# Performance work log

Hardware: AMD Instinct MI355X
Metric: run time of the kernel (lower is better)

Reference implementation:

```python
import jax, jax.numpy as jnp
import numpy as np
from jax import lax

B, T, O, E, I = 256, 16, 32, 32, 32
H, HL = 64, 64  # edge_dim, latent_edge_dim
TE, EI = T * E, E + I


def _mlp(x, layers):
    for w, b in layers[:-1]:
        x = jax.nn.relu(x @ w + b)
    w, b = layers[-1]
    return x @ w + b


def _get_edges(x, layers):
    # x: [B, O, D]; antisymmetric pairwise aggregation over upper-triangular pairs
    Bn, On, D = x.shape
    ii, jj = np.triu_indices(On, 1)  # static indices, P = O(O-1)/2
    pair_in = jnp.concatenate([x[:, ii, :], x[:, jj, :]], axis=-1)  # [B, P, 2D]
    e = _mlp(pair_in, layers)  # [B, P, H_out]
    agg = jnp.zeros((Bn, On, e.shape[-1]), x.dtype)
    agg = agg.at[:, ii, :].add(e).at[:, jj, :].add(-e)
    return agg


def setup_inputs() -> dict:
    key = jax.random.key(0)
    ks = iter(jax.random.split(key, 64))

    def lin(din, dout):
        w = jax.random.normal(next(ks), (din, dout), jnp.float32) * (1.0 / np.sqrt(din)).astype(np.float32)
        b = jnp.zeros((dout,), jnp.float32)
        return w, b

    inp = {"z_explicit_seq": jax.random.normal(next(ks), (B, T, O, E), jnp.float32)}
    groups = {
        "ee": [(2 * TE, 64), (64, 64), (64, H)],
        "ne": [(TE + H, 64), (64, 64), (64, 32), (32, I)],
        "le": [(2 * EI, 64), (64, 64), (64, HL)],
        "lt": [(EI + HL, 64), (64, 64), (64, 32), (32, 16), (16, EI)],
    }
    for name, dims in groups.items():
        for k, (din, dout) in enumerate(dims, start=1):
            w, b = lin(din, dout)
            inp[f"{name}{k}_w"] = w
            inp[f"{name}{k}_b"] = b
    inp["t_future"] = 8
    return inp


def reference(z_explicit_seq,
              ee1_w, ee1_b, ee2_w, ee2_b, ee3_w, ee3_b,
              ne1_w, ne1_b, ne2_w, ne2_b, ne3_w, ne3_b, ne4_w, ne4_b,
              le1_w, le1_b, le2_w, le2_b, le3_w, le3_b,
              lt1_w, lt1_b, lt2_w, lt2_b, lt3_w, lt3_b, lt4_w, lt4_b, lt5_w, lt5_b,
              t_future):
    ee = [(ee1_w, ee1_b), (ee2_w, ee2_b), (ee3_w, ee3_b)]
    ne = [(ne1_w, ne1_b), (ne2_w, ne2_b), (ne3_w, ne3_b), (ne4_w, ne4_b)]
    le = [(le1_w, le1_b), (le2_w, le2_b), (le3_w, le3_b)]
    lt = [(lt1_w, lt1_b), (lt2_w, lt2_b), (lt3_w, lt3_b), (lt4_w, lt4_b), (lt5_w, lt5_b)]

    z = z_explicit_seq  # [B, T, O, E]
    # define_source: first frame + temporal diffs, flatten time into features
    src = jnp.concatenate([z[:, :1], z[:, 1:] - z[:, :-1]], axis=1)  # [B,T,O,E]
    src = jnp.transpose(src, (0, 2, 1, 3)).reshape(B, O, TE)  # [B,O,TE]

    edge_agg = _get_edges(src, ee)  # [B,O,H]
    z_impl = _mlp(jnp.concatenate([src, edge_agg], axis=-1), ne)  # [B,O,I]
    z_cur = jnp.concatenate([z[:, -1], z_impl], axis=-1)  # [B,O,EI]

    def step(zc, _):
        agg = _get_edges(zc, le)  # [B,O,HL]
        delta = _mlp(jnp.concatenate([zc, agg], axis=-1), lt)  # [B,O,EI]
        zn = zc + delta
        return zn, zn[..., :E]

    _, preds = lax.scan(step, z_cur, None, length=t_future)  # [t,B,O,E]
    return jnp.transpose(preds, (1, 0, 2, 3))  # [B,t_future,O,E]
```

## Files before the change

kernel.cpp:

```cpp
#include <hip/hip_runtime.h>

#define NB 256
#define NO 32
#define NEE 32
#define NT 16
#define THREADS 512

typedef const float* __restrict__ fp;

struct Params {
  fp z;
  fp ee1w, ee1b, ee2w, ee2b, ee3w, ee3b;
  fp ne1w, ne1b, ne2w, ne2b, ne3w, ne3b, ne4w, ne4b;
  fp le1w, le1b, le2w, le2b, le3w, le3b;
  fp lt1w, lt1b, lt2w, lt2b, lt3w, lt3b, lt4w, lt4b, lt5w, lt5b;
  float* out;
  int tf;
};

__device__ __forceinline__ float frelu(float x) { return x > 0.f ? x : 0.f; }

__device__ __forceinline__ float rl(float v, int l) {
  return __uint_as_float(__builtin_amdgcn_readlane(__float_as_uint(v), l));
}

#define OFF_UT  0
#define OFF_VT  2112
#define OFF_AG  4224
#define OFF_BN  6272
#define OFF_NW  8320
#define LDSF    16000

__device__ __forceinline__ void stageN(float* dst, const float* __restrict__ src,
                                       int nf4, int tid) {
  for (int i4 = tid; i4 < nf4; i4 += THREADS)
    *(float4*)(dst + i4 * 4) = *(const float4*)(src + i4 * 4);
}

template<int KC>
__device__ __forceinline__ void dense4L(const float* x0, const float* x1,
                                        const float* x2, const float* x3,
                                        const float* __restrict__ w, int ldw,
                                        int col, float o[4]) {
#pragma unroll 4
  for (int kc = 0; kc < KC; ++kc) {
    float w0 = w[(4 * kc + 0) * ldw + col];
    float w1 = w[(4 * kc + 1) * ldw + col];
    float w2 = w[(4 * kc + 2) * ldw + col];
    float w3 = w[(4 * kc + 3) * ldw + col];
    float4 a = *(const float4*)(x0 + 4 * kc);
    float4 b = *(const float4*)(x1 + 4 * kc);
    float4 c = *(const float4*)(x2 + 4 * kc);
    float4 d = *(const float4*)(x3 + 4 * kc);
    o[0] = fmaf(a.x, w0, o[0]); o[0] = fmaf(a.y, w1, o[0]); o[0] = fmaf(a.z, w2, o[0]); o[0] = fmaf(a.w, w3, o[0]);
    o[1] = fmaf(b.x, w0, o[1]); o[1] = fmaf(b.y, w1, o[1]); o[1] = fmaf(b.z, w2, o[1]); o[1] = fmaf(b.w, w3, o[1]);
    o[2] = fmaf(c.x, w0, o[2]); o[2] = fmaf(c.y, w1, o[2]); o[2] = fmaf(c.z, w2, o[2]); o[2] = fmaf(c.w, w3, o[2]);
    o[3] = fmaf(d.x, w0, o[3]); o[3] = fmaf(d.y, w1, o[3]); o[3] = fmaf(d.z, w2, o[3]); o[3] = fmaf(d.w, w3, o[3]);
  }
}

__global__ __attribute__((amdgpu_waves_per_eu(2)))
__launch_bounds__(THREADS) void rld_kernel(Params P) {
  __shared__ float lds[LDSF];
  const int b = blockIdx.x;
  const int tid = (int)threadIdx.x;
  const int lane = tid & 63;
  const int wave = tid >> 6;
  const int cc = lane & 31;
  const int c16 = lane & 15;

  float* UT = lds + OFF_UT;
  float* VT = lds + OFF_VT;
  float* AG = lds + OFF_AG;
  float* sBn = lds + OFF_BN + wave * 256;
  float* src = lds + OFF_BN;
  const float* wlt2 = lds + OFF_NW;
  const float* wlt3 = lds + OFF_NW + 4096;
  const float* wlt4 = lds + OFF_NW + 6144;
  const float* wlt5 = lds + OFF_NW + 6656;
  const int i0 = wave, i1 = wave + 8, i2 = wave + 16, i3 = wave + 24;
  const int h33 = lane * 33;
  const float* zb = P.z + (size_t)b * NT * NO * NEE;

  stageN(lds + OFF_NW,        P.lt2w, 1024, tid);
  stageN(lds + OFF_NW + 4096, P.lt3w,  512, tid);
  stageN(lds + OFF_NW + 6144, P.lt4w,  128, tid);
  stageN(lds + OFF_NW + 6656, P.lt5w,  256, tid);

  float au[4] = {0,0,0,0}, av[4] = {0,0,0,0}, s1r[4] = {0,0,0,0};
  for (int qq = 0; qq < 8; ++qq) {
    __syncthreads();
    for (int idx = tid; idx < 2048; idx += THREADS) {
      int i = idx >> 6, kk = idx & 63;
      int k = qq * 64 + kk, t = k >> 5, e = k & 31;
      float v = zb[(t * NO + i) * NEE + e];
      if (t > 0) v -= zb[((t - 1) * NO + i) * NEE + e];
      src[i * 64 + kk] = v;
    }
    __syncthreads();
    for (int c = 0; c < 2; ++c) {
      int r0 = qq * 64 + c * 32;
      const float* x0 = src + i0 * 64 + c * 32;
      const float* x1 = src + i1 * 64 + c * 32;
      const float* x2 = src + i2 * 64 + c * 32;
      const float* x3 = src + i3 * 64 + c * 32;
      dense4L<8>(x0, x1, x2, x3, P.ee1w + (size_t)r0 * 64,         64, lane, au);
      dense4L<8>(x0, x1, x2, x3, P.ee1w + (size_t)(512 + r0) * 64, 64, lane, av);
      dense4L<8>(x0, x1, x2, x3, P.ne1w + (size_t)r0 * 64,         64, lane, s1r);
    }
  }
  {
    float eb1 = P.ee1b[lane];
    UT[h33 + i0] = au[0] + eb1; UT[h33 + i1] = au[1] + eb1;
    UT[h33 + i2] = au[2] + eb1; UT[h33 + i3] = au[3] + eb1;
    VT[h33 + i0] = av[0]; VT[h33 + i1] = av[1];
    VT[h33 + i2] = av[2]; VT[h33 + i3] = av[3];
  }
  for (int z = tid; z < 2048; z += THREADS) AG[z] = 0.f;

  float w2c[64], w3c[64];
#pragma unroll
  for (int h = 0; h < 64; ++h) w2c[h] = P.ee2w[h * 64 + lane];
#pragma unroll
  for (int h = 0; h < 64; ++h) w3c[h] = P.ee3w[h * 64 + lane];
  float b2c = P.ee2b[lane], b3c = P.ee3b[lane];
  __syncthreads();

  const int tf = P.tf;
  float zci[4] = {0, 0, 0, 0};
  float* outb = P.out + (size_t)b * tf * NO * NEE;

  for (int s = 0; s <= tf; ++s) {
    {
      int pi = 0, rem = wave * 62;
      while (rem >= 31 - pi) { rem -= 31 - pi; ++pi; }
      int pj = pi + 1 + rem;
#pragma unroll 1
      for (int pp = 0; pp < 31; ++pp) {
        const int iA = pi, jA = pj;
        ++pj; if (pj == 32) { ++pi; pj = pi + 1; }
        const int iB = pi, jB = pj;
        ++pj; if (pj == 32) { ++pi; pj = pi + 1; }
        float xA = fmaxf(UT[h33 + iA] + VT[h33 + jA], 0.f);
        float xB = fmaxf(UT[h33 + iB] + VT[h33 + jB], 0.f);
        float a0 = b2c, a1 = 0.f, c0 = b2c, c1 = 0.f;
#pragma unroll
        for (int h = 0; h < 64; h += 2) {
          a0 = fmaf(rl(xA, h),     w2c[h],     a0);
          a1 = fmaf(rl(xA, h + 1), w2c[h + 1], a1);
          c0 = fmaf(rl(xB, h),     w2c[h],     c0);
          c1 = fmaf(rl(xB, h + 1), w2c[h + 1], c1);
        }
        float yA = fmaxf(a0 + a1, 0.f);
        float yB = fmaxf(c0 + c1, 0.f);
        float e0 = b3c, e1 = 0.f, f0 = b3c, f1 = 0.f;
#pragma unroll
        for (int h = 0; h < 64; h += 2) {
          e0 = fmaf(rl(yA, h),     w3c[h],     e0);
          e1 = fmaf(rl(yA, h + 1), w3c[h + 1], e1);
          f0 = fmaf(rl(yB, h),     w3c[h],     f0);
          f1 = fmaf(rl(yB, h + 1), w3c[h + 1], f1);
        }
        float eA = e0 + e1, eB = f0 + f1;
        atomicAdd(&AG[iA * 64 + lane],  eA);
        atomicAdd(&AG[jA * 64 + lane], -eA);
        atomicAdd(&AG[iB * 64 + lane],  eB);
        atomicAdd(&AG[jB * 64 + lane], -eB);
      }
    }
    __syncthreads();

    if (s == 0) {
      float nb1 = P.ne1b[lane], nb2 = P.ne2b[lane];
      float nb3 = P.ne3b[cc],   nb4 = P.ne4b[cc];
      float o1[4] = {s1r[0] + nb1, s1r[1] + nb1, s1r[2] + nb1, s1r[3] + nb1};
      dense4L<16>(AG + i0 * 64, AG + i1 * 64, AG + i2 * 64, AG + i3 * 64,
                  P.ne1w + (size_t)512 * 64, 64, lane, o1);
      sBn[lane] = frelu(o1[0]); sBn[64 + lane] = frelu(o1[1]);
      sBn[128 + lane] = frelu(o1[2]); sBn[192 + lane] = frelu(o1[3]);
      float o2[4] = {nb2, nb2, nb2, nb2};
      dense4L<16>(sBn, sBn + 64, sBn + 128, sBn + 192, P.ne2w, 64, lane, o2);
      sBn[lane] = frelu(o2[0]); sBn[64 + lane] = frelu(o2[1]);
      sBn[128 + lane] = frelu(o2[2]); sBn[192 + lane] = frelu(o2[3]);
      float o3[4] = {nb3, nb3, nb3, nb3};
      dense4L<16>(sBn, sBn + 64, sBn + 128, sBn + 192, P.ne3w, 32, cc, o3);
      sBn[cc] = frelu(o3[0]); sBn[64 + cc] = frelu(o3[1]);
      sBn[128 + cc] = frelu(o3[2]); sBn[192 + cc] = frelu(o3[3]);
      float o4[4] = {nb4, nb4, nb4, nb4};
      dense4L<8>(sBn, sBn + 64, sBn + 128, sBn + 192, P.ne4w, 32, cc, o4);
      zci[0] = (lane < 32) ? zb[(15 * NO + i0) * NEE + lane] : o4[0];
      zci[1] = (lane < 32) ? zb[(15 * NO + i1) * NEE + lane] : o4[1];
      zci[2] = (lane < 32) ? zb[(15 * NO + i2) * NEE + lane] : o4[2];
      zci[3] = (lane < 32) ? zb[(15 * NO + i3) * NEE + lane] : o4[3];
    } else {
      float lb1 = P.lt1b[lane], lb2 = P.lt2b[lane];
      float lb3 = P.lt3b[cc],   lb4 = P.lt4b[c16], lb5 = P.lt5b[lane];
      float o1[4] = {lb1, lb1, lb1, lb1};
      dense4L<16>(sBn, sBn + 64, sBn + 128, sBn + 192, P.lt1w, 64, lane, o1);
      dense4L<16>(AG + i0 * 64, AG + i1 * 64, AG + i2 * 64, AG + i3 * 64,
                  P.lt1w + (size_t)64 * 64, 64, lane, o1);
      sBn[lane] = frelu(o1[0]); sBn[64 + lane] = frelu(o1[1]);
      sBn[128 + lane] = frelu(o1[2]); sBn[192 + lane] = frelu(o1[3]);
      float o2[4] = {lb2, lb2, lb2, lb2};
      dense4L<16>(sBn, sBn + 64, sBn + 128, sBn + 192, wlt2, 64, lane, o2);
      sBn[lane] = frelu(o2[0]); sBn[64 + lane] = frelu(o2[1]);
      sBn[128 + lane] = frelu(o2[2]); sBn[192 + lane] = frelu(o2[3]);
      float o3[4] = {lb3, lb3, lb3, lb3};
      dense4L<16>(sBn, sBn + 64, sBn + 128, sBn + 192, wlt3, 32, cc, o3);
      sBn[cc] = frelu(o3[0]); sBn[64 + cc] = frelu(o3[1]);
      sBn[128 + cc] = frelu(o3[2]); sBn[192 + cc] = frelu(o3[3]);
      float o4[4] = {lb4, lb4, lb4, lb4};
      dense4L<8>(sBn, sBn + 64, sBn + 128, sBn + 192, wlt4, 16, c16, o4);
      sBn[c16] = frelu(o4[0]); sBn[64 + c16] = frelu(o4[1]);
      sBn[128 + c16] = frelu(o4[2]); sBn[192 + c16] = frelu(o4[3]);
      float o5[4] = {lb5, lb5, lb5, lb5};
      dense4L<4>(sBn, sBn + 64, sBn + 128, sBn + 192, wlt5, 64, lane, o5);
      zci[0] += o5[0]; zci[1] += o5[1]; zci[2] += o5[2]; zci[3] += o5[3];
      int t = s - 1;
      if (lane < 32) {
        outb[(t * NO + i0) * NEE + lane] = zci[0];
        outb[(t * NO + i1) * NEE + lane] = zci[1];
        outb[(t * NO + i2) * NEE + lane] = zci[2];
        outb[(t * NO + i3) * NEE + lane] = zci[3];
      }
    }
    __syncthreads();

    if (s < tf) {
      if (s == 0) {
#pragma unroll
        for (int h = 0; h < 64; ++h) w2c[h] = P.le2w[h * 64 + lane];
#pragma unroll
        for (int h = 0; h < 64; ++h) w3c[h] = P.le3w[h * 64 + lane];
        b2c = P.le2b[lane]; b3c = P.le3b[lane];
      }
      for (int z = tid; z < 2048; z += THREADS) AG[z] = 0.f;
      sBn[lane] = zci[0]; sBn[64 + lane] = zci[1];
      sBn[128 + lane] = zci[2]; sBn[192 + lane] = zci[3];
      float gb1 = P.le1b[lane];
      float ou[4] = {0,0,0,0}, ov[4] = {0,0,0,0};
      dense4L<16>(sBn, sBn + 64, sBn + 128, sBn + 192, P.le1w,        64, lane, ou);
      dense4L<16>(sBn, sBn + 64, sBn + 128, sBn + 192, P.le1w + 4096, 64, lane, ov);
      UT[h33 + i0] = ou[0] + gb1; UT[h33 + i1] = ou[1] + gb1;
      UT[h33 + i2] = ou[2] + gb1; UT[h33 + i3] = ou[3] + gb1;
      VT[h33 + i0] = ov[0]; VT[h33 + i1] = ov[1];
      VT[h33 + i2] = ov[2]; VT[h33 + i3] = ov[3];
    }
    __syncthreads();
  }
}

extern "C" void kernel_launch(void* const* d_in, const int* in_sizes, int n_in,
                              void* d_out, int out_size, void* d_ws, size_t ws_size,
                              hipStream_t stream) {
  (void)in_sizes; (void)n_in; (void)d_ws; (void)ws_size;
  Params P;
  int q = 0;
  P.z    = (fp)d_in[q++];
  P.ee1w = (fp)d_in[q++]; P.ee1b = (fp)d_in[q++];
  P.ee2w = (fp)d_in[q++]; P.ee2b = (fp)d_in[q++];
  P.ee3w = (fp)d_in[q++]; P.ee3b = (fp)d_in[q++];
  P.ne1w = (fp)d_in[q++]; P.ne1b = (fp)d_in[q++];
  P.ne2w = (fp)d_in[q++]; P.ne2b = (fp)d_in[q++];
  P.ne3w = (fp)d_in[q++]; P.ne3b = (fp)d_in[q++];
  P.ne4w = (fp)d_in[q++]; P.ne4b = (fp)d_in[q++];
  P.le1w = (fp)d_in[q++]; P.le1b = (fp)d_in[q++];
  P.le2w = (fp)d_in[q++]; P.le2b = (fp)d_in[q++];
  P.le3w = (fp)d_in[q++]; P.le3b = (fp)d_in[q++];
  P.lt1w = (fp)d_in[q++]; P.lt1b = (fp)d_in[q++];
  P.lt2w = (fp)d_in[q++]; P.lt2b = (fp)d_in[q++];
  P.lt3w = (fp)d_in[q++]; P.lt3b = (fp)d_in[q++];
  P.lt4w = (fp)d_in[q++]; P.lt4b = (fp)d_in[q++];
  P.lt5w = (fp)d_in[q++]; P.lt5b = (fp)d_in[q++];
  P.out = (float*)d_out;
  P.tf = out_size / (NB * NO * NEE);
  if (P.tf < 1) P.tf = 1;
  hipLaunchKernelGGL(rld_kernel, dim3(NB), dim3(THREADS), 0, stream, P);
}
```

Baseline: 1.179 ms.

## Stream edge MLP weights through one register slot per batch of eight pairs

Replaces the two persistent 64-entry register weight arrays with a single 64-entry slot. Each batch of 8 pairs reloads the layer-2 column from global memory, computes layer 2 for all 8 pairs, then reloads the slot with the layer-3 column. The waves_per_eu(2) hint is dropped, and work is padded to 64 pair slots per wave with masked atomics for the unused ones. This lowers register pressure so more waves can be resident, at the cost of repeated global/L2 weight loads and some wasted padded compute.

```diff
diff --git a/kernel.cpp b/kernel.cpp
--- a/kernel.cpp
+++ b/kernel.cpp
@@ -59,8 +59,7 @@
   }
 }
 
-__global__ __attribute__((amdgpu_waves_per_eu(2)))
-__launch_bounds__(THREADS) void rld_kernel(Params P) {
+__global__ __launch_bounds__(THREADS) void rld_kernel(Params P) {
   __shared__ float lds[LDSF];
   const int b = blockIdx.x;
   const int tid = (int)threadIdx.x;
@@ -118,11 +117,6 @@
   }
   for (int z = tid; z < 2048; z += THREADS) AG[z] = 0.f;
 
-  float w2c[64], w3c[64];
-#pragma unroll
-  for (int h = 0; h < 64; ++h) w2c[h] = P.ee2w[h * 64 + lane];
-#pragma unroll
-  for (int h = 0; h < 64; ++h) w3c[h] = P.ee3w[h * 64 + lane];
   float b2c = P.ee2b[lane], b3c = P.ee3b[lane];
   __syncthreads();
 
@@ -132,40 +126,57 @@
 
   for (int s = 0; s <= tf; ++s) {
     {
-      int pi = 0, rem = wave * 62;
+      fp w2p = s ? P.le2w : P.ee2w;
+      fp w3p = s ? P.le3w : P.ee3w;
+      int pi = 0, rem = wave * 64;
       while (rem >= 31 - pi) { rem -= 31 - pi; ++pi; }
       int pj = pi + 1 + rem;
+      int rank = wave * 64;
+      float wslot[64];
 #pragma unroll 1
-      for (int pp = 0; pp < 31; ++pp) {
-        const int iA = pi, jA = pj;
-        ++pj; if (pj == 32) { ++pi; pj = pi + 1; }
-        const int iB = pi, jB = pj;
-        ++pj; if (pj == 32) { ++pi; pj = pi + 1; }
-        float xA = fmaxf(UT[h33 + iA] + VT[h33 + jA], 0.f);
-        float xB = fmaxf(UT[h33 + iB] + VT[h33 + jB], 0.f);
-        float a0 = b2c, a1 = 0.f, c0 = b2c, c1 = 0.f;
-#pragma unroll
-        for (int h = 0; h < 64; h += 2) {
-          a0 = fmaf(rl(xA, h),     w2c[h],     a0);
-          a1 = fmaf(rl(xA, h + 1), w2c[h + 1], a1);
-          c0 = fmaf(rl(xB, h),     w2c[h],     c0);
-          c1 = fmaf(rl(xB, h + 1), w2c[h + 1], c1);
+      for (int bt = 0; bt < 8; ++bt) {
+        __builtin_amdgcn_sched_barrier(0);
+#pragma unroll
+        for (int h = 0; h < 64; ++h) wslot[h] = w2p[h * 64 + lane];
+        int ii[8], jj[8]; bool rr[8];
+        float x[8];
+#pragma unroll
+        for (int q = 0; q < 8; ++q) {
+          bool real = (rank < 496);
+          rr[q] = real;
+          ii[q] = real ? pi : 0; jj[q] = real ? pj : 0;
+          if (real) { ++pj; if (pj == 32) { ++pi; pj = pi + 1; } }
+          ++rank;
+          x[q] = fmaxf(UT[h33 + ii[q]] + VT[h33 + jj[q]], 0.f);
         }
-        float yA = fmaxf(a0 + a1, 0.f);
-        float yB = fmaxf(c0 + c1, 0.f);
-        float e0 = b3c, e1 = 0.f, f0 = b3c, f1 = 0.f;
-#pragma unroll
-        for (int h = 0; h < 64; h += 2) {
-          e0 = fmaf(rl(yA, h),     w3c[h],     e0);
-          e1 = fmaf(rl(yA, h + 1), w3c[h + 1], e1);
-          f0 = fmaf(rl(yB, h),     w3c[h],     f0);
-          f1 = fmaf(rl(yB, h + 1), w3c[h + 1], f1);
+        float Y[8];
+#pragma unroll
+        for (int q = 0; q < 8; ++q) {
+          float a0 = b2c, a1 = 0.f;
+#pragma unroll
+          for (int h = 0; h < 64; h += 2) {
+            a0 = fmaf(rl(x[q], h),     wslot[h],     a0);
+            a1 = fmaf(rl(x[q], h + 1), wslot[h + 1], a1);
+          }
+          Y[q] = fmaxf(a0 + a1, 0.f);
         }
-        float eA = e0 + e1, eB = f0 + f1;
-        atomicAdd(&AG[iA * 64 + lane],  eA);
-        atomicAdd(&AG[jA * 64 + lane], -eA);
-        atomicAdd(&AG[iB * 64 + lane],  eB);
-        atomicAdd(&AG[jB * 64 + lane], -eB);
+        __builtin_amdgcn_sched_barrier(0);
+#pragma unroll
+        for (int h = 0; h < 64; ++h) wslot[h] = w3p[h * 64 + lane];
+#pragma unroll
+        for (int q = 0; q < 8; ++q) {
+          float e0 = b3c, e1 = 0.f;
+#pragma unroll
+          for (int h = 0; h < 64; h += 2) {
+            e0 = fmaf(rl(Y[q], h),     wslot[h],     e0);
+            e1 = fmaf(rl(Y[q], h + 1), wslot[h + 1], e1);
+          }
+          if (rr[q]) {
+            float e = e0 + e1;
+            atomicAdd(&AG[ii[q] * 64 + lane],  e);
+            atomicAdd(&AG[jj[q] * 64 + lane], -e);
+          }
+        }
       }
     }
     __syncthreads();
@@ -228,10 +239,6 @@
 
     if (s < tf) {
       if (s == 0) {
-#pragma unroll
-        for (int h = 0; h < 64; ++h) w2c[h] = P.le2w[h * 64 + lane];
-#pragma unroll
-        for (int h = 0; h < 64; ++h) w3c[h] = P.le3w[h * 64 + lane];
         b2c = P.le2b[lane]; b3c = P.le3b[lane];
       }
       for (int z = tid; z < 2048; z += THREADS) AG[z] = 0.f;
```

After: 2.460 ms. 109% more time.
